# Optimization experiments

Measured on AMD Instinct MI355X. Metric: run time of the kernel, lower is better.

The kernel has to match this reference:

```python
import jax, jax.numpy as jnp
import numpy as np

DIM = 512
HEADS = 8
DIM_HEAD = 32
INNER = HEADS * DIM_HEAD  # 256
B, N = 2, 2048
EPS = 1e-5


def setup_inputs() -> dict:
    key = jax.random.key(0)
    ks = jax.random.split(key, 6)
    x = jax.random.normal(ks[0], (B, N, DIM), dtype=jnp.float32)
    rel_pos_bias = jax.random.normal(ks[1], (HEADS, N, N), dtype=jnp.float32)
    ln_scale = jnp.ones((DIM,), dtype=jnp.float32)
    w_qkv = jax.random.normal(ks[2], (DIM, INNER * 3), dtype=jnp.float32) / np.sqrt(DIM)
    w_out = jax.random.normal(ks[3], (INNER, DIM), dtype=jnp.float32) / np.sqrt(INNER)
    b_out = jnp.zeros((DIM,), dtype=jnp.float32)
    return {"x": x, "rel_pos_bias": rel_pos_bias, "ln_scale": ln_scale,
            "w_qkv": w_qkv, "w_out": w_out, "b_out": b_out}


def reference(x, rel_pos_bias, ln_scale, w_qkv, w_out, b_out):
    scale = DIM_HEAD ** -0.5
    # LayerNorm (no bias), eps=1e-5
    mu = jnp.mean(x, axis=-1, keepdims=True)
    var = jnp.mean(jnp.square(x - mu), axis=-1, keepdims=True)
    xn = (x - mu) * jax.lax.rsqrt(var + EPS) * ln_scale
    # fused QKV projection, no bias
    qkv = xn @ w_qkv  # [b, n, 3*inner]
    q, k, v = jnp.split(qkv, 3, axis=-1)
    def to_heads(t):
        b, n, _ = t.shape
        return t.reshape(b, n, HEADS, DIM_HEAD).transpose(0, 2, 1, 3)  # b h n d
    q, k, v = map(to_heads, (q, k, v))
    q = q * scale
    sim = jnp.einsum('bhid,bhjd->bhij', q, k)
    sim = sim + rel_pos_bias  # (h,n,n) broadcasts over batch
    attn = jax.nn.softmax(sim, axis=-1)
    o = jnp.einsum('bhij,bhjd->bhid', attn, v)
    o = o.transpose(0, 2, 1, 3).reshape(x.shape[0], x.shape[1], INNER)  # b n (h d)
    return o @ w_out + b_out
```

## Files before the change

kernel.cpp:

```cpp
#include <hip/hip_runtime.h>
#include <hip/hip_bf16.h>
#include <cstdint>

#define NB 2
#define NSEQ 2048
#define NDIM 512
#define NHEAD 8
#define DHEAD 32
#define NINNER 256
#define NQKV 768
#define LNEPS 1e-5f
#define QSCALE 0.17677669529663687f

typedef short short8 __attribute__((ext_vector_type(8)));
typedef float f32x4 __attribute__((ext_vector_type(4)));
typedef unsigned int u32x4 __attribute__((ext_vector_type(4)));
typedef unsigned int u32x2 __attribute__((ext_vector_type(2)));
typedef unsigned short u16;
typedef unsigned int u32;

__device__ __forceinline__ f32x4 mfma16(short8 a, short8 b, f32x4 c) {
    return __builtin_amdgcn_mfma_f32_16x16x32_bf16(a, b, c, 0, 0, 0);
}

__device__ __forceinline__ u16 f2bf(float a) {
    union { float f; u32 u; } x; x.f = a;
    u32 r = x.u + 0x7fffu + ((x.u >> 16) & 1u);
    return (u16)(r >> 16);
}
__device__ __forceinline__ float bf2f(u16 h) {
    union { float f; u32 u; } x; x.u = ((u32)h) << 16; return x.f;
}
__device__ __forceinline__ void split2(float a, u16& hi, u16& lo) {
    hi = f2bf(a);
    lo = f2bf(a - bf2f(hi));
}
__device__ __forceinline__ u32 pk2(float a, float b) {
    return (u32)f2bf(a) | ((u32)f2bf(b) << 16);
}

__global__ __launch_bounds__(256) void ln_kernel(
    const float* __restrict__ x, const float* __restrict__ gamma,
    u32* __restrict__ xn_hi, u32* __restrict__ xn_lo)
{
    const int row = blockIdx.x;
    const int t = threadIdx.x;
    const float2 v = ((const float2*)(x + (size_t)row * NDIM))[t];
    float s1 = v.x + v.y;
    float s2 = v.x * v.x + v.y * v.y;
    #pragma unroll
    for (int off = 32; off >= 1; off >>= 1) {
        s1 += __shfl_down(s1, off);
        s2 += __shfl_down(s2, off);
    }
    __shared__ float a1[4], a2[4];
    if ((t & 63) == 0) { a1[t >> 6] = s1; a2[t >> 6] = s2; }
    __syncthreads();
    const float ts1 = a1[0] + a1[1] + a1[2] + a1[3];
    const float ts2 = a2[0] + a2[1] + a2[2] + a2[3];
    const float mu = ts1 * (1.0f / NDIM);
    const float var = ts2 * (1.0f / NDIM) - mu * mu;
    const float rs = rsqrtf(var + LNEPS);
    const float2 g = ((const float2*)gamma)[t];
    u16 h0, l0, h1, l1;
    split2((v.x - mu) * rs * g.x, h0, l0);
    split2((v.y - mu) * rs * g.y, h1, l1);
    xn_hi[(size_t)row * (NDIM / 2) + t] = (u32)h0 | ((u32)h1 << 16);
    xn_lo[(size_t)row * (NDIM / 2) + t] = (u32)l0 | ((u32)l1 << 16);
}

__global__ __launch_bounds__(256) void wtrans_kernel(
    const float* __restrict__ wq, u16* __restrict__ wqT_hi, u16* __restrict__ wqT_lo,
    const float* __restrict__ wo, u16* __restrict__ woT_hi, u16* __restrict__ woT_lo)
{
    __shared__ __align__(16) u16 th[64][72], tl[64][72];
    const int t = threadIdx.x;
    const float* w; u16 *wT_hi, *wT_lo; int K, N, k0, n0;
    if (blockIdx.x < 96) {
        w = wq; wT_hi = wqT_hi; wT_lo = wqT_lo; K = NDIM; N = NQKV;
        k0 = (blockIdx.x & 7) * 64; n0 = (blockIdx.x >> 3) * 64;
    } else {
        const int b = blockIdx.x - 96;
        w = wo; wT_hi = woT_hi; wT_lo = woT_lo; K = NINNER; N = NDIM;
        k0 = (b & 3) * 64; n0 = (b >> 2) * 64;
    }
    {
        const int k = t >> 2, c = (t & 3) * 16;
        const float* src = w + (size_t)(k0 + k) * N + n0 + c;
        #pragma unroll
        for (int jj = 0; jj < 4; jj++) {
            const f32x4 w4 = *(const f32x4*)(src + jj * 4);
            #pragma unroll
            for (int e = 0; e < 4; e++) {
                u16 hh, ll;
                split2(w4[e], hh, ll);
                th[k][c + jj * 4 + e] = hh;
                tl[k][c + jj * 4 + e] = ll;
            }
        }
    }
    __syncthreads();
    {
        const int n = t >> 2, kc = (t & 3) * 16;
        u16 hb[16], lb[16];
        #pragma unroll
        for (int j = 0; j < 16; j++) { hb[j] = th[kc + j][n]; lb[j] = tl[kc + j][n]; }
        u16* dh = wT_hi + (size_t)(n0 + n) * K + k0 + kc;
        u16* dl = wT_lo + (size_t)(n0 + n) * K + k0 + kc;
        *(short8*)dh = *(short8*)hb;
        *(short8*)(dh + 8) = *(short8*)(hb + 8);
        *(short8*)dl = *(short8*)lb;
        *(short8*)(dl + 8) = *(short8*)(lb + 8);
    }
}

__global__ __launch_bounds__(256) void vtrans_kernel(
    const u16* __restrict__ v, u16* __restrict__ vt)
{
    __shared__ __align__(16) u16 sh[64][40];
    const int t = threadIdx.x;
    const int n0 = blockIdx.x * 64;
    const int bh = blockIdx.y;
    {
        const int n = t >> 2, c = (t & 3) * 8;
        *(short8*)&sh[n][c] = *(const short8*)(v + ((size_t)bh * NSEQ + n0 + n) * DHEAD + c);
    }
    __syncthreads();
    {
        const int d = t >> 3, nc = (t & 7) * 8;
        u16 buf[8];
        #pragma unroll
        for (int j = 0; j < 8; j++) buf[j] = sh[nc + j][d];
        *(short8*)(vt + ((size_t)bh * DHEAD + d) * NSEQ + n0 + nc) = *(short8*)buf;
    }
}

__global__ __launch_bounds__(256, 4) void qkv_kernel(
    const u16* __restrict__ xn_hi, const u16* __restrict__ xn_lo,
    const u16* __restrict__ wT_hi, const u16* __restrict__ wT_lo,
    u16* __restrict__ q_hi, u16* __restrict__ q_lo,
    u16* __restrict__ k_hi, u16* __restrict__ k_lo,
    u16* __restrict__ v)
{
    __shared__ __align__(16) u16 Ah[64][40], Al[64][40], Bh[64][40], Bl[64][40];
    const int t = threadIdx.x;
    const int wave = t >> 6, lane = t & 63;
    const int lrow = lane & 15, lquad = lane >> 4;
    const int rowBase = blockIdx.x * 64;
    const int colBase = blockIdx.y * 64;
    const int wm = (wave & 1) * 32;
    const int wn = (wave >> 1) * 32;
    const int kf = lquad * 8;
    const f32x4 zero = {0.f, 0.f, 0.f, 0.f};
    f32x4 acc[2][2];
    acc[0][0] = zero; acc[0][1] = zero; acc[1][0] = zero; acc[1][1] = zero;

    const int sr = t >> 2, sc = (t & 3) * 8;

    for (int k0 = 0; k0 < NDIM; k0 += 32) {
        __syncthreads();
        *(short8*)&Ah[sr][sc] = *(const short8*)(xn_hi + (size_t)(rowBase + sr) * NDIM + k0 + sc);
        *(short8*)&Al[sr][sc] = *(const short8*)(xn_lo + (size_t)(rowBase + sr) * NDIM + k0 + sc);
        *(short8*)&Bh[sr][sc] = *(const short8*)(wT_hi + (size_t)(colBase + sr) * NDIM + k0 + sc);
        *(short8*)&Bl[sr][sc] = *(const short8*)(wT_lo + (size_t)(colBase + sr) * NDIM + k0 + sc);
        __syncthreads();
        const short8 a0h = *(const short8*)&Ah[wm + lrow][kf];
        const short8 a0l = *(const short8*)&Al[wm + lrow][kf];
        const short8 a1h = *(const short8*)&Ah[wm + 16 + lrow][kf];
        const short8 a1l = *(const short8*)&Al[wm + 16 + lrow][kf];
        const short8 b0h = *(const short8*)&Bh[wn + lrow][kf];
        const short8 b0l = *(const short8*)&Bl[wn + lrow][kf];
        const short8 b1h = *(const short8*)&Bh[wn + 16 + lrow][kf];
        const short8 b1l = *(const short8*)&Bl[wn + 16 + lrow][kf];
        acc[0][0] = mfma16(a0h, b0h, acc[0][0]); acc[0][0] = mfma16(a0h, b0l, acc[0][0]); acc[0][0] = mfma16(a0l, b0h, acc[0][0]);
        acc[0][1] = mfma16(a0h, b1h, acc[0][1]); acc[0][1] = mfma16(a0h, b1l, acc[0][1]); acc[0][1] = mfma16(a0l, b1h, acc[0][1]);
        acc[1][0] = mfma16(a1h, b0h, acc[1][0]); acc[1][0] = mfma16(a1h, b0l, acc[1][0]); acc[1][0] = mfma16(a1l, b0h, acc[1][0]);
        acc[1][1] = mfma16(a1h, b1h, acc[1][1]); acc[1][1] = mfma16(a1h, b1l, acc[1][1]); acc[1][1] = mfma16(a1l, b1h, acc[1][1]);
    }

    #pragma unroll
    for (int mi = 0; mi < 2; mi++) {
        #pragma unroll
        for (int ni = 0; ni < 2; ni++) {
            #pragma unroll
            for (int r = 0; r < 4; r++) {
                const int grow = rowBase + wm + mi * 16 + lquad * 4 + r;
                const int gcol = colBase + wn + ni * 16 + lrow;
                const float val = acc[mi][ni][r];
                const int bidx = grow >> 11;
                const int n = grow & (NSEQ - 1);
                const int sec = gcol >> 8;
                const int idx = gcol & 255;
                const int head = idx >> 5, d = idx & 31;
                const int bh = bidx * NHEAD + head;
                if (sec == 0) {
                    u16 hh, ll;
                    split2(val * QSCALE, hh, ll);
                    const size_t a = ((size_t)bh * NSEQ + n) * DHEAD + d;
                    q_hi[a] = hh; q_lo[a] = ll;
                } else if (sec == 1) {
                    u16 hh, ll;
                    split2(val, hh, ll);
                    const size_t a = ((size_t)bh * NSEQ + n) * DHEAD + d;
                    k_hi[a] = hh; k_lo[a] = ll;
                } else {
                    v[((size_t)bh * NSEQ + n) * DHEAD + d] = f2bf(val);
                }
            }
        }
    }
}

__global__ __launch_bounds__(512, 4) void attn_kernel(
    const u16* __restrict__ q_hi, const u16* __restrict__ q_lo,
    const u16* __restrict__ k_hi, const u16* __restrict__ k_lo,
    const u16* __restrict__ vt,
    const float* __restrict__ bias,
    u16* __restrict__ o_hi, u16* __restrict__ o_lo)
{
    __shared__ __align__(16) float cA[2][2][4][64][4];
    __shared__ __align__(16) float cB[2][2][4][64][4];
    __shared__ float cl[2][2][4][16];
    const int t = threadIdx.x;
    const int wave = t >> 6, lane = t & 63;
    const int lrow = lane & 15, lquad = lane >> 4;
    const int qpair = wave & 1, kslice = wave >> 1;
    const int bh = blockIdx.y;
    const int batch = bh >> 3, head = bh & 7;
    const int qb = blockIdx.x * 64 + qpair * 32;
    const size_t qkb = (size_t)bh * NSEQ * DHEAD;
    const size_t qoff0 = (size_t)(qb + lrow) * DHEAD + lquad * 8;
    const size_t qoff1 = (size_t)(qb + 16 + lrow) * DHEAD + lquad * 8;
    const short8 qh0 = *(const short8*)(q_hi + qkb + qoff0);
    const short8 ql0 = *(const short8*)(q_lo + qkb + qoff0);
    const short8 qh1 = *(const short8*)(q_hi + qkb + qoff1);
    const short8 ql1 = *(const short8*)(q_lo + qkb + qoff1);
    const f32x4 zero = {0.f, 0.f, 0.f, 0.f};
    f32x4 accA0 = zero, accB0 = zero, accA1 = zero, accB1 = zero;
    float lp0 = 0.f, lp1 = 0.f;
    const int kperm = ((lrow >> 2) << 3) | (lrow & 3);
    const float* bptr0 = bias + (size_t)head * NSEQ * NSEQ + (size_t)(qb + lrow) * NSEQ;
    const float* bptr1 = bptr0 + 16 * NSEQ;
    const int kt0 = kslice * 512;

    short8 kv[2][6];
    f32x4 bs[2][4];

#define KVLOAD(idx, p) do { \
        const int kt_ = kt0 + (idx) * 32; \
        const size_t kof_ = (size_t)(kt_ + kperm) * DHEAD + lquad * 8; \
        kv[p][0] = *(const short8*)(k_hi + qkb + kof_); \
        kv[p][1] = *(const short8*)(k_lo + qkb + kof_); \
        kv[p][2] = *(const short8*)(k_hi + qkb + kof_ + 4 * DHEAD); \
        kv[p][3] = *(const short8*)(k_lo + qkb + kof_ + 4 * DHEAD); \
        kv[p][4] = *(const short8*)(vt + qkb + (size_t)lrow * NSEQ + kt_ + lquad * 8); \
        kv[p][5] = *(const short8*)(vt + qkb + (size_t)(16 + lrow) * NSEQ + kt_ + lquad * 8); \
    } while (0)

#define BLOAD(idx, p) do { \
        const int kt_ = kt0 + (idx) * 32; \
        bs[p][0] = *(const f32x4*)(bptr0 + kt_ + lquad * 8); \
        bs[p][1] = *(const f32x4*)(bptr0 + kt_ + lquad * 8 + 4); \
        bs[p][2] = *(const f32x4*)(bptr1 + kt_ + lquad * 8); \
        bs[p][3] = *(const f32x4*)(bptr1 + kt_ + lquad * 8 + 4); \
    } while (0)

    KVLOAD(0, 0);
    BLOAD(0, 0);
    BLOAD(1, 1);

    #pragma unroll
    for (int i = 0; i < 16; i++) {
        const int cur = i & 1;
        const int nxt = cur ^ 1;
        if (i < 15) KVLOAD(i + 1, nxt);

        {
            f32x4 c0 = zero, c1 = zero;
            c0 = mfma16(kv[cur][0], qh0, c0); c0 = mfma16(kv[cur][0], ql0, c0); c0 = mfma16(kv[cur][1], qh0, c0);
            c1 = mfma16(kv[cur][2], qh0, c1); c1 = mfma16(kv[cur][2], ql0, c1); c1 = mfma16(kv[cur][3], qh0, c1);
            f32x4 p0, p1;
            #pragma unroll
            for (int r = 0; r < 4; r++) {
                p0[r] = __expf(c0[r] + bs[cur][0][r]);
                p1[r] = __expf(c1[r] + bs[cur][1][r]);
            }
            lp0 += (p0[0] + p0[1]) + (p0[2] + p0[3]) + (p1[0] + p1[1]) + (p1[2] + p1[3]);
            union { u32x4 u; short8 s; } cv;
            cv.u[0] = pk2(p0[0], p0[1]);
            cv.u[1] = pk2(p0[2], p0[3]);
            cv.u[2] = pk2(p1[0], p1[1]);
            cv.u[3] = pk2(p1[2], p1[3]);
            accA0 = mfma16(kv[cur][4], cv.s, accA0);
            accB0 = mfma16(kv[cur][5], cv.s, accB0);
        }
        {
            f32x4 c0 = zero, c1 = zero;
            c0 = mfma16(kv[cur][0], qh1, c0); c0 = mfma16(kv[cur][0], ql1, c0); c0 = mfma16(kv[cur][1], qh1, c0);
            c1 = mfma16(kv[cur][2], qh1, c1); c1 = mfma16(kv[cur][2], ql1, c1); c1 = mfma16(kv[cur][3], qh1, c1);
            f32x4 p0, p1;
            #pragma unroll
            for (int r = 0; r < 4; r++) {
                p0[r] = __expf(c0[r] + bs[cur][2][r]);
                p1[r] = __expf(c1[r] + bs[cur][3][r]);
            }
            lp1 += (p0[0] + p0[1]) + (p0[2] + p0[3]) + (p1[0] + p1[1]) + (p1[2] + p1[3]);
            union { u32x4 u; short8 s; } cv;
            cv.u[0] = pk2(p0[0], p0[1]);
            cv.u[1] = pk2(p0[2], p0[3]);
            cv.u[2] = pk2(p1[0], p1[1]);
            cv.u[3] = pk2(p1[2], p1[3]);
            accA1 = mfma16(kv[cur][4], cv.s, accA1);
            accB1 = mfma16(kv[cur][5], cv.s, accB1);
        }
        if (i < 14) BLOAD(i + 2, cur);
    }
#undef KVLOAD
#undef BLOAD

    lp0 += __shfl_xor(lp0, 16); lp0 += __shfl_xor(lp0, 32);
    lp1 += __shfl_xor(lp1, 16); lp1 += __shfl_xor(lp1, 32);

    *(f32x4*)&cA[qpair][0][kslice][lane][0] = accA0;
    *(f32x4*)&cB[qpair][0][kslice][lane][0] = accB0;
    *(f32x4*)&cA[qpair][1][kslice][lane][0] = accA1;
    *(f32x4*)&cB[qpair][1][kslice][lane][0] = accB1;
    if (lquad == 0) {
        cl[qpair][0][kslice][lrow] = lp0;
        cl[qpair][1][kslice][lrow] = lp1;
    }
    __syncthreads();
    if (wave < 4) {
        const int qp = wave >> 1, s = wave & 1;
        f32x4 sA = *(const f32x4*)&cA[qp][s][0][lane][0];
        f32x4 sB = *(const f32x4*)&cB[qp][s][0][lane][0];
        #pragma unroll
        for (int w = 1; w < 4; w++) {
            sA += *(const f32x4*)&cA[qp][s][w][lane][0];
            sB += *(const f32x4*)&cB[qp][s][w][lane][0];
        }
        const float lt = cl[qp][s][0][lrow] + cl[qp][s][1][lrow]
                       + cl[qp][s][2][lrow] + cl[qp][s][3][lrow];
        const float inv = 1.0f / lt;
        const int q = blockIdx.x * 64 + qp * 32 + s * 16 + lrow;
        const size_t base = ((size_t)batch * NSEQ + q) * NINNER + head * DHEAD + lquad * 4;
        u16 h[8], l[8];
        #pragma unroll
        for (int r = 0; r < 4; r++) {
            split2(sA[r] * inv, h[r], l[r]);
            split2(sB[r] * inv, h[4 + r], l[4 + r]);
        }
        *(u32x2*)&o_hi[base] = *(u32x2*)&h[0];
        *(u32x2*)&o_hi[base + 16] = *(u32x2*)&h[4];
        *(u32x2*)&o_lo[base] = *(u32x2*)&l[0];
        *(u32x2*)&o_lo[base + 16] = *(u32x2*)&l[4];
    }
}

__global__ __launch_bounds__(256, 4) void out_kernel(
    const u16* __restrict__ o_hi, const u16* __restrict__ o_lo,
    const u16* __restrict__ wT_hi, const u16* __restrict__ wT_lo,
    const float* __restrict__ b_out,
    float* __restrict__ out)
{
    __shared__ __align__(16) u16 Ah[64][40], Al[64][40], Bh[64][40], Bl[64][40];
    const int t = threadIdx.x;
    const int wave = t >> 6, lane = t & 63;
    const int lrow = lane & 15, lquad = lane >> 4;
    const int rowBase = blockIdx.x * 64;
    const int colBase = blockIdx.y * 64;
    const int wm = (wave & 1) * 32;
    const int wn = (wave >> 1) * 32;
    const int kf = lquad * 8;
    const f32x4 zero = {0.f, 0.f, 0.f, 0.f};
    f32x4 acc[2][2];
    acc[0][0] = zero; acc[0][1] = zero; acc[1][0] = zero; acc[1][1] = zero;

    const int sr = t >> 2, sc = (t & 3) * 8;

    for (int k0 = 0; k0 < NINNER; k0 += 32) {
        __syncthreads();
        *(short8*)&Ah[sr][sc] = *(const short8*)(o_hi + (size_t)(rowBase + sr) * NINNER + k0 + sc);
        *(short8*)&Al[sr][sc] = *(const short8*)(o_lo + (size_t)(rowBase + sr) * NINNER + k0 + sc);
        *(short8*)&Bh[sr][sc] = *(const short8*)(wT_hi + (size_t)(colBase + sr) * NINNER + k0 + sc);
        *(short8*)&Bl[sr][sc] = *(const short8*)(wT_lo + (size_t)(colBase + sr) * NINNER + k0 + sc);
        __syncthreads();
        const short8 a0h = *(const short8*)&Ah[wm + lrow][kf];
        const short8 a0l = *(const short8*)&Al[wm + lrow][kf];
        const short8 a1h = *(const short8*)&Ah[wm + 16 + lrow][kf];
        const short8 a1l = *(const short8*)&Al[wm + 16 + lrow][kf];
        const short8 b0h = *(const short8*)&Bh[wn + lrow][kf];
        const short8 b0l = *(const short8*)&Bl[wn + lrow][kf];
        const short8 b1h = *(const short8*)&Bh[wn + 16 + lrow][kf];
        const short8 b1l = *(const short8*)&Bl[wn + 16 + lrow][kf];
        acc[0][0] = mfma16(a0h, b0h, acc[0][0]); acc[0][0] = mfma16(a0h, b0l, acc[0][0]); acc[0][0] = mfma16(a0l, b0h, acc[0][0]);
        acc[0][1] = mfma16(a0h, b1h, acc[0][1]); acc[0][1] = mfma16(a0h, b1l, acc[0][1]); acc[0][1] = mfma16(a0l, b1h, acc[0][1]);
        acc[1][0] = mfma16(a1h, b0h, acc[1][0]); acc[1][0] = mfma16(a1h, b0l, acc[1][0]); acc[1][0] = mfma16(a1l, b0h, acc[1][0]);
        acc[1][1] = mfma16(a1h, b1h, acc[1][1]); acc[1][1] = mfma16(a1h, b1l, acc[1][1]); acc[1][1] = mfma16(a1l, b1h, acc[1][1]);
    }

    #pragma unroll
    for (int mi = 0; mi < 2; mi++) {
        #pragma unroll
        for (int ni = 0; ni < 2; ni++) {
            #pragma unroll
            for (int r = 0; r < 4; r++) {
                const int grow = rowBase + wm + mi * 16 + lquad * 4 + r;
                const int gcol = colBase + wn + ni * 16 + lrow;
                out[(size_t)grow * NDIM + gcol] = acc[mi][ni][r] + b_out[gcol];
            }
        }
    }
}

extern "C" void kernel_launch(void* const* d_in, const int* in_sizes, int n_in,
                              void* d_out, int out_size, void* d_ws, size_t ws_size,
                              hipStream_t stream)
{
    (void)in_sizes; (void)n_in; (void)out_size; (void)ws_size;
    const float* x     = (const float*)d_in[0];
    const float* bias  = (const float*)d_in[1];
    const float* gamma = (const float*)d_in[2];
    const float* wqkv  = (const float*)d_in[3];
    const float* wout  = (const float*)d_in[4];
    const float* bout  = (const float*)d_in[5];
    float* out = (float*)d_out;

    char* ws = (char*)d_ws;
    size_t off = 0;
    auto carve = [&](size_t bytes) -> void* {
        void* p = (void*)(ws + off);
        off += (bytes + 255) & ~(size_t)255;
        return p;
    };
    const size_t rows = (size_t)NB * NSEQ;
    const size_t hn = (size_t)NB * NHEAD * NSEQ * DHEAD;
    u16* xn_hi = (u16*)carve(rows * NDIM * 2);
    u16* xn_lo = (u16*)carve(rows * NDIM * 2);
    u16* wqT_hi = (u16*)carve((size_t)NQKV * NDIM * 2);
    u16* wqT_lo = (u16*)carve((size_t)NQKV * NDIM * 2);
    u16* woT_hi = (u16*)carve((size_t)NDIM * NINNER * 2);
    u16* woT_lo = (u16*)carve((size_t)NDIM * NINNER * 2);
    u16* q_hi  = (u16*)carve(hn * 2);
    u16* q_lo  = (u16*)carve(hn * 2);
    u16* k_hi  = (u16*)carve(hn * 2);
    u16* k_lo  = (u16*)carve(hn * 2);
    u16* vbuf  = (u16*)carve(hn * 2);
    u16* vt    = (u16*)carve(hn * 2);
    u16* o_hi  = (u16*)carve(rows * NINNER * 2);
    u16* o_lo  = (u16*)carve(rows * NINNER * 2);

    ln_kernel<<<dim3((unsigned)rows), 256, 0, stream>>>(x, gamma, (u32*)xn_hi, (u32*)xn_lo);
    wtrans_kernel<<<dim3(128), 256, 0, stream>>>(wqkv, wqT_hi, wqT_lo, wout, woT_hi, woT_lo);
    qkv_kernel<<<dim3(64, 12), 256, 0, stream>>>(xn_hi, xn_lo, wqT_hi, wqT_lo,
                                                 q_hi, q_lo, k_hi, k_lo, vbuf);
    vtrans_kernel<<<dim3(NSEQ / 64, NB * NHEAD), 256, 0, stream>>>(vbuf, vt);
    attn_kernel<<<dim3(32, 16), 512, 0, stream>>>(q_hi, q_lo, k_hi, k_lo,
                                                  vt, bias, o_hi, o_lo);
    out_kernel<<<dim3(64, 8), 256, 0, stream>>>(o_hi, o_lo, woT_hi, woT_lo, bout, out);
}
```

Before: 276.6 us.

## Split attention key range across 8 waves per 32-query block, doubling grid

After: 280.1 us. No clear change (+1.3%).

```diff
diff --git a/kernel.cpp b/kernel.cpp
--- a/kernel.cpp
+++ b/kernel.cpp
@@ -218,16 +218,16 @@
     const float* __restrict__ bias,
     u16* __restrict__ o_hi, u16* __restrict__ o_lo)
 {
-    __shared__ __align__(16) float cA[2][2][4][64][4];
-    __shared__ __align__(16) float cB[2][2][4][64][4];
-    __shared__ float cl[2][2][4][16];
+    __shared__ __align__(16) float cA[2][8][64][4];
+    __shared__ __align__(16) float cB[2][8][64][4];
+    __shared__ float cl[2][8][16];
     const int t = threadIdx.x;
     const int wave = t >> 6, lane = t & 63;
     const int lrow = lane & 15, lquad = lane >> 4;
-    const int qpair = wave & 1, kslice = wave >> 1;
+    const int kslice = wave;
     const int bh = blockIdx.y;
     const int batch = bh >> 3, head = bh & 7;
-    const int qb = blockIdx.x * 64 + qpair * 32;
+    const int qb = blockIdx.x * 32;
     const size_t qkb = (size_t)bh * NSEQ * DHEAD;
     const size_t qoff0 = (size_t)(qb + lrow) * DHEAD + lquad * 8;
     const size_t qoff1 = (size_t)(qb + 16 + lrow) * DHEAD + lquad * 8;
@@ -241,7 +241,7 @@
     const int kperm = ((lrow >> 2) << 3) | (lrow & 3);
     const float* bptr0 = bias + (size_t)head * NSEQ * NSEQ + (size_t)(qb + lrow) * NSEQ;
     const float* bptr1 = bptr0 + 16 * NSEQ;
-    const int kt0 = kslice * 512;
+    const int kt0 = kslice * 256;
 
     short8 kv[2][6];
     f32x4 bs[2][4];
@@ -270,10 +270,10 @@
     BLOAD(1, 1);
 
     #pragma unroll
-    for (int i = 0; i < 16; i++) {
+    for (int i = 0; i < 8; i++) {
         const int cur = i & 1;
         const int nxt = cur ^ 1;
-        if (i < 15) KVLOAD(i + 1, nxt);
+        if (i < 7) KVLOAD(i + 1, nxt);
 
         {
             f32x4 c0 = zero, c1 = zero;
@@ -313,7 +313,7 @@
             accA1 = mfma16(kv[cur][4], cv.s, accA1);
             accB1 = mfma16(kv[cur][5], cv.s, accB1);
         }
-        if (i < 14) BLOAD(i + 2, cur);
+        if (i < 6) BLOAD(i + 2, cur);
     }
 #undef KVLOAD
 #undef BLOAD
@@ -321,39 +321,37 @@
     lp0 += __shfl_xor(lp0, 16); lp0 += __shfl_xor(lp0, 32);
     lp1 += __shfl_xor(lp1, 16); lp1 += __shfl_xor(lp1, 32);
 
-    *(f32x4*)&cA[qpair][0][kslice][lane][0] = accA0;
-    *(f32x4*)&cB[qpair][0][kslice][lane][0] = accB0;
-    *(f32x4*)&cA[qpair][1][kslice][lane][0] = accA1;
-    *(f32x4*)&cB[qpair][1][kslice][lane][0] = accB1;
+    *(f32x4*)&cA[0][kslice][lane][0] = accA0;
+    *(f32x4*)&cB[0][kslice][lane][0] = accB0;
+    *(f32x4*)&cA[1][kslice][lane][0] = accA1;
+    *(f32x4*)&cB[1][kslice][lane][0] = accB1;
     if (lquad == 0) {
-        cl[qpair][0][kslice][lrow] = lp0;
-        cl[qpair][1][kslice][lrow] = lp1;
+        cl[0][kslice][lrow] = lp0;
+        cl[1][kslice][lrow] = lp1;
     }
     __syncthreads();
     if (wave < 4) {
-        const int qp = wave >> 1, s = wave & 1;
-        f32x4 sA = *(const f32x4*)&cA[qp][s][0][lane][0];
-        f32x4 sB = *(const f32x4*)&cB[qp][s][0][lane][0];
-        #pragma unroll
-        for (int w = 1; w < 4; w++) {
-            sA += *(const f32x4*)&cA[qp][s][w][lane][0];
-            sB += *(const f32x4*)&cB[qp][s][w][lane][0];
-        }
-        const float lt = cl[qp][s][0][lrow] + cl[qp][s][1][lrow]
-                       + cl[qp][s][2][lrow] + cl[qp][s][3][lrow];
+        const int s = wave >> 1, part = wave & 1;
+        const float (*src)[64][4] = part ? (const float (*)[64][4])cB[s]
+                                         : (const float (*)[64][4])cA[s];
+        f32x4 sv = *(const f32x4*)&src[0][lane][0];
+        #pragma unroll
+        for (int w = 1; w < 8; w++) {
+            sv += *(const f32x4*)&src[w][lane][0];
+        }
+        float lt = 0.f;
+        #pragma unroll
+        for (int w = 0; w < 8; w++) lt += cl[s][w][lrow];
         const float inv = 1.0f / lt;
-        const int q = blockIdx.x * 64 + qp * 32 + s * 16 + lrow;
-        const size_t base = ((size_t)batch * NSEQ + q) * NINNER + head * DHEAD + lquad * 4;
-        u16 h[8], l[8];
+        const int q = qb + s * 16 + lrow;
+        const size_t base = ((size_t)batch * NSEQ + q) * NINNER + head * DHEAD + part * 16 + lquad * 4;
+        u16 h[4], l[4];
         #pragma unroll
         for (int r = 0; r < 4; r++) {
-            split2(sA[r] * inv, h[r], l[r]);
-            split2(sB[r] * inv, h[4 + r], l[4 + r]);
+            split2(sv[r] * inv, h[r], l[r]);
         }
         *(u32x2*)&o_hi[base] = *(u32x2*)&h[0];
-        *(u32x2*)&o_hi[base + 16] = *(u32x2*)&h[4];
         *(u32x2*)&o_lo[base] = *(u32x2*)&l[0];
-        *(u32x2*)&o_lo[base + 16] = *(u32x2*)&l[4];
     }
 }
 
@@ -455,7 +453,7 @@
     qkv_kernel<<<dim3(64, 12), 256, 0, stream>>>(xn_hi, xn_lo, wqT_hi, wqT_lo,
                                                  q_hi, q_lo, k_hi, k_lo, vbuf);
     vtrans_kernel<<<dim3(NSEQ / 64, NB * NHEAD), 256, 0, stream>>>(vbuf, vt);
-    attn_kernel<<<dim3(32, 16), 512, 0, stream>>>(q_hi, q_lo, k_hi, k_lo,
-                                                  vt, bias, o_hi, o_lo);
+    attn_kernel<<<dim3(NSEQ / 32, NB * NHEAD), 512, 0, stream>>>(q_hi, q_lo, k_hi, k_lo,
+                                                                 vt, bias, o_hi, o_lo);
     out_kernel<<<dim3(64, 8), 256, 0, stream>>>(o_hi, o_lo, woT_hi, woT_lo, bout, out);
 }
```
